# Kernel tuning notes

Hardware: AMD Instinct MI355X
Metric: run time of the kernel (lower is better)

Reference implementation:

```python
import jax, jax.numpy as jnp
import numpy as np

EPS = 1e-12  # tf.contrib layer_norm default epsilon
FORGET_BIAS = 1.0  # tf LSTMCell default


def _layer_norm(x, gamma, beta):
    mu = jnp.mean(x, axis=-1, keepdims=True)
    var = jnp.mean(jnp.square(x - mu), axis=-1, keepdims=True)
    return (x - mu) * jax.lax.rsqrt(var + EPS) * gamma + beta


def setup_inputs() -> dict:
    key = jax.random.key(0)
    ks = jax.random.split(key, 16)
    B, T, OBS, ACT, H = 256, 512, 256, 64, 64
    N = B * T
    s = 0.05
    inp = {
        "obs": jax.random.normal(ks[0], (N, OBS), jnp.float32),
        "action": jax.random.normal(ks[1], (N, ACT), jnp.float32),
        "c0": jnp.zeros((B, H), jnp.float32),
        "h0": jnp.zeros((B, H), jnp.float32),
        "W_obs": jax.random.normal(ks[2], (OBS, H), jnp.float32) * s,
        "b_obs": jnp.zeros((H,), jnp.float32),
        "g1": jnp.ones((H,), jnp.float32),
        "beta1": jnp.zeros((H,), jnp.float32),
        "W_act": jax.random.normal(ks[3], (ACT, H), jnp.float32) * s,
        "b_act": jnp.zeros((H,), jnp.float32),
        "g2": jnp.ones((H,), jnp.float32),
        "beta2": jnp.zeros((H,), jnp.float32),
        "W_lstm": jax.random.normal(ks[4], (2 * H + H, 4 * H), jnp.float32) * s,
        "b_lstm": jnp.zeros((4 * H,), jnp.float32),
        "g3": jnp.ones((H,), jnp.float32),
        "beta3": jnp.zeros((H,), jnp.float32),
        "W_out": jax.random.uniform(ks[5], (H, 1), jnp.float32, -0.003, 0.003),
        "b_out": jnp.zeros((1,), jnp.float32),
        "batch_size": B,
        "step_size": T,
    }
    return inp


def reference(obs, action, c0, h0, W_obs, b_obs, g1, beta1, W_act, b_act, g2, beta2,
              W_lstm, b_lstm, g3, beta3, W_out, b_out, batch_size, step_size):
    H = 64
    # obs branch (output is overwritten below — faithful to source bug)
    x = jnp.maximum(_layer_norm(obs @ W_obs + b_obs, g1, beta1), 0.0)
    # action branch
    yd = action @ W_act + b_act
    x = _layer_norm(yd, g2, beta2)  # BUG in source: overwrites obs branch
    y = jnp.maximum(yd, 0.0)
    xy = jnp.concatenate([x, y], axis=-1)  # [B*T, 128]
    rnn_in = xy.reshape(batch_size, step_size, 2 * H).transpose(1, 0, 2)  # [T,B,128]

    def step(carry, x_t):
        c, h = carry
        z = jnp.concatenate([x_t, h], axis=-1) @ W_lstm + b_lstm  # [B,4H]
        i, j, f, o = jnp.split(z, 4, axis=-1)  # tf LSTMCell gate order
        c_new = c * jax.nn.sigmoid(f + FORGET_BIAS) + jax.nn.sigmoid(i) * jnp.tanh(j)
        h_new = jax.nn.sigmoid(o) * jnp.tanh(c_new)
        return (c_new, h_new), h_new

    (c_fin, h_fin), hs = jax.lax.scan(step, (c0, h0), rnn_in)  # hs: [T,B,H]
    out = hs.transpose(1, 0, 2).reshape(batch_size * step_size, H)
    out = _layer_norm(out, g3, beta3)
    q = out @ W_out + b_out  # [B*T, 1]
    return q, c_fin, h_fin
```

## Files before the change

kernel.cpp:

```cpp
#include <hip/hip_runtime.h>

#define HD 64
#define TT 512
#define BB 256
#define NROWS (BB * TT)

__device__ __forceinline__ float rl(float v, int k) {
  return __uint_as_float(__builtin_amdgcn_readlane(__float_as_uint(v), k));
}
__device__ __forceinline__ float wsum(float v) {
#pragma unroll
  for (int m = 32; m >= 1; m >>= 1) v += __shfl_xor(v, m, 64);
  return v;
}
__device__ __forceinline__ float sigmoidf_(float x) {
  return 1.0f / (1.0f + __expf(-x));
}
__device__ __forceinline__ float tanhf_(float x) {
  return 1.0f - 2.0f / (__expf(2.0f * x) + 1.0f);
}
__device__ __forceinline__ unsigned short f2bf(float f) {
  unsigned int u = __float_as_uint(f);
  u = (u + 0x7fffu + ((u >> 16) & 1u)) >> 16;
  return (unsigned short)u;
}
__device__ __forceinline__ float ldz(const float* p) { return *p; }
__device__ __forceinline__ float ldz(const unsigned short* p) {
  return __uint_as_float(((unsigned int)(*p)) << 16);
}
__device__ __forceinline__ void store8(float* p, float4 a, float4 b) {
  *(float4*)p = a;
  *(float4*)(p + 4) = b;
}
__device__ __forceinline__ void store8(unsigned short* p, float4 a, float4 b) {
  union { unsigned short us[8]; int4 v; } u;
  u.us[0] = f2bf(a.x); u.us[1] = f2bf(a.y); u.us[2] = f2bf(a.z); u.us[3] = f2bf(a.w);
  u.us[4] = f2bf(b.x); u.us[5] = f2bf(b.y); u.us[6] = f2bf(b.z); u.us[7] = f2bf(b.w);
  *(int4*)p = u.v;
}
__device__ __forceinline__ float4 fma4(float4 a, float s, float4 w) {
  a.x += s * w.x; a.y += s * w.y; a.z += s * w.z; a.w += s * w.w;
  return a;
}
__device__ __forceinline__ float4 add4(float4 a, float4 b) {
  a.x += b.x; a.y += b.y; a.z += b.z; a.w += b.w;
  return a;
}

template <typename ZT>
__global__ __launch_bounds__(256) void kA(const float* __restrict__ act,
                                          const float* __restrict__ Wact,
                                          const float* __restrict__ bact,
                                          const float* __restrict__ g2,
                                          const float* __restrict__ beta2,
                                          const float* __restrict__ Wl,
                                          const float* __restrict__ bl,
                                          ZT* __restrict__ Zx) {
  __shared__ float xy[64][128];
  const int tid = threadIdx.x;
  const int lane = tid & 63;
  const int wv = tid >> 6;
  const int r0blk = blockIdx.x * 64;

  float wreg[64];
#pragma unroll
  for (int k = 0; k < 64; ++k) wreg[k] = Wact[k * 64 + lane];
  const float ba = bact[lane], gg = g2[lane], bb = beta2[lane];

  for (int i = 0; i < 16; ++i) {
    const int r = i * 4 + wv;
    const int row = r0blk + r;
    const float a = act[row * 64 + lane];
    float yd = ba;
#pragma unroll
    for (int k = 0; k < 64; ++k) yd += rl(a, k) * wreg[k];
    const float mu = wsum(yd) * (1.0f / 64.0f);
    const float d = yd - mu;
    const float var = wsum(d * d) * (1.0f / 64.0f);
    const float x = d * rsqrtf(var + 1e-12f) * gg + bb;
    xy[r][lane] = x;
    xy[r][64 + lane] = fmaxf(yd, 0.0f);
  }
  __syncthreads();

  const int tc = tid & 31;
  const int tr = tid >> 5;
  const int c0 = tc * 8;
  float4 accA[8], accB[8];
#pragma unroll
  for (int r = 0; r < 8; ++r) {
    accA[r] = make_float4(0.f, 0.f, 0.f, 0.f);
    accB[r] = make_float4(0.f, 0.f, 0.f, 0.f);
  }
  for (int kk = 0; kk < 128; kk += 4) {
    float4 xv[8];
#pragma unroll
    for (int r = 0; r < 8; ++r) xv[r] = *(const float4*)&xy[tr * 8 + r][kk];
#pragma unroll
    for (int dk = 0; dk < 4; ++dk) {
      const float4 wa = *(const float4*)&Wl[(kk + dk) * 256 + c0];
      const float4 wb = *(const float4*)&Wl[(kk + dk) * 256 + c0 + 4];
#pragma unroll
      for (int r = 0; r < 8; ++r) {
        const float xr = (dk == 0) ? xv[r].x : (dk == 1) ? xv[r].y : (dk == 2) ? xv[r].z : xv[r].w;
        accA[r] = fma4(accA[r], xr, wa);
        accB[r] = fma4(accB[r], xr, wb);
      }
    }
  }
  const float4 bla = *(const float4*)&bl[c0];
  const float4 blb = *(const float4*)&bl[c0 + 4];
#pragma unroll
  for (int r = 0; r < 8; ++r) {
    const int row = r0blk + tr * 8 + r;
    store8(&Zx[(size_t)row * 256 + c0], add4(accA[r], bla), add4(accB[r], blb));
  }
}

template <typename ZT>
__global__ __launch_bounds__(256) void kB(const ZT* __restrict__ Zx,
                                          const float* __restrict__ Wl,
                                          const float* __restrict__ c0p,
                                          const float* __restrict__ h0p,
                                          float* __restrict__ hs,
                                          float* __restrict__ cfin,
                                          float* __restrict__ hfin) {
  __shared__ float zbuf[2][256];
  const int tid = threadIdx.x;
  const int m = tid & 63;
  const int b = blockIdx.x;

  float wcol[64];
#pragma unroll
  for (int k = 0; k < 64; ++k) wcol[k] = Wl[(128 + k) * 256 + tid];

  float c = c0p[b * 64 + m];
  float h = h0p[b * 64 + m];

  const ZT* zrow = Zx + (size_t)b * TT * 256;
  float* hsrow = hs + (size_t)b * TT * 64;

  float p0 = ldz(&zrow[0 * 256 + tid]);
  float p1 = ldz(&zrow[1 * 256 + tid]);
  float p2 = ldz(&zrow[2 * 256 + tid]);
  float p3 = ldz(&zrow[3 * 256 + tid]);

#define STEP(PZ, T)                                                        \
  {                                                                        \
    float a0 = 0.f, a1 = 0.f, a2 = 0.f, a3 = 0.f;                          \
    _Pragma("unroll") for (int k = 0; k < 64; k += 4) {                    \
      a0 += rl(h, k) * wcol[k];                                            \
      a1 += rl(h, k + 1) * wcol[k + 1];                                    \
      a2 += rl(h, k + 2) * wcol[k + 2];                                    \
      a3 += rl(h, k + 3) * wcol[k + 3];                                    \
    }                                                                      \
    const float zv = PZ + ((a0 + a1) + (a2 + a3));                         \
    zbuf[(T)&1][tid] = zv;                                                 \
    int tn = (T) + 4;                                                      \
    if (tn > TT - 1) tn = TT - 1;                                          \
    PZ = ldz(&zrow[(size_t)tn * 256 + tid]);                               \
    asm volatile("s_waitcnt lgkmcnt(0)\n\ts_barrier" ::: "memory");        \
    const float zi = zbuf[(T)&1][m];                                       \
    const float zj = zbuf[(T)&1][64 + m];                                  \
    const float zf = zbuf[(T)&1][128 + m];                                 \
    const float zo = zbuf[(T)&1][192 + m];                                 \
    c = c * sigmoidf_(zf + 1.0f) + sigmoidf_(zi) * tanhf_(zj);             \
    h = sigmoidf_(zo) * tanhf_(c);                                         \
    if (tid < 64) hsrow[(T)*64 + m] = h;                                   \
  }

  for (int t = 0; t < TT; t += 4) {
    STEP(p0, t)
    STEP(p1, t + 1)
    STEP(p2, t + 2)
    STEP(p3, t + 3)
  }
#undef STEP

  if (tid < 64) {
    cfin[b * 64 + m] = c;
    hfin[b * 64 + m] = h;
  }
}

__global__ __launch_bounds__(256) void kC(const float* __restrict__ hs,
                                          const float* __restrict__ g3,
                                          const float* __restrict__ beta3,
                                          const float* __restrict__ Wout,
                                          const float* __restrict__ bout,
                                          float* __restrict__ q) {
  const int lane = threadIdx.x & 63;
  const int wv = threadIdx.x >> 6;
  const float g = g3[lane], be = beta3[lane], wo = Wout[lane], bo = bout[0];
  for (int n = blockIdx.x * 4 + wv; n < NROWS; n += gridDim.x * 4) {
    const float v = hs[(size_t)n * 64 + lane];
    const float mu = wsum(v) * (1.0f / 64.0f);
    const float d = v - mu;
    const float var = wsum(d * d) * (1.0f / 64.0f);
    const float xn = d * rsqrtf(var + 1e-12f) * g + be;
    const float s = wsum(xn * wo);
    if (lane == 0) q[n] = s + bo;
  }
}

extern "C" void kernel_launch(void* const* d_in, const int* in_sizes, int n_in,
                              void* d_out, int out_size, void* d_ws, size_t ws_size,
                              hipStream_t stream) {
  const float* action = (const float*)d_in[1];
  const float* c0 = (const float*)d_in[2];
  const float* h0 = (const float*)d_in[3];
  const float* Wact = (const float*)d_in[8];
  const float* bact = (const float*)d_in[9];
  const float* g2 = (const float*)d_in[10];
  const float* b2 = (const float*)d_in[11];
  const float* Wl = (const float*)d_in[12];
  const float* bl = (const float*)d_in[13];
  const float* g3 = (const float*)d_in[14];
  const float* b3 = (const float*)d_in[15];
  const float* Wout = (const float*)d_in[16];
  const float* bout = (const float*)d_in[17];

  float* q = (float*)d_out;
  float* cfin = q + NROWS;
  float* hfin = cfin + BB * HD;

  const size_t zx32 = (size_t)NROWS * 256 * sizeof(float);
  const size_t zx16 = (size_t)NROWS * 256 * sizeof(unsigned short);
  const size_t hsb = (size_t)NROWS * 64 * sizeof(float);

  if (ws_size >= zx32 + hsb) {
    float* Zx = (float*)d_ws;
    float* hs = (float*)((char*)d_ws + zx32);
    kA<float><<<NROWS / 64, 256, 0, stream>>>(action, Wact, bact, g2, b2, Wl, bl, Zx);
    kB<float><<<BB, 256, 0, stream>>>(Zx, Wl, c0, h0, hs, cfin, hfin);
    kC<<<2048, 256, 0, stream>>>(hs, g3, b3, Wout, bout, q);
  } else {
    unsigned short* Zx = (unsigned short*)d_ws;
    float* hs = (float*)((char*)d_ws + zx16);
    kA<unsigned short><<<NROWS / 64, 256, 0, stream>>>(action, Wact, bact, g2, b2, Wl, bl, Zx);
    kB<unsigned short><<<BB, 256, 0, stream>>>(Zx, Wl, c0, h0, hs, cfin, hfin);
    kC<<<2048, 256, 0, stream>>>(hs, g3, b3, Wout, bout, q);
  }
}
```

Baseline: 417.0 us.

## Run LSTM recurrence on one wavefront per batch using bf16 MFMA

The recurrent kernel drops from four wavefronts per batch element, which used readlane dot products and a block barrier each step, to a single wavefront. That wavefront computes the h·W_hh product with bf16 16x16x32 MFMA instructions, with the weights held in registers as bf16 fragments. This removes the cross-wave barrier and LDS gate exchange on the serial critical path. The cost is bf16 rounding of h and the weights, extra MFMAs whose results are mostly discarded (only row 0 is used), and fewer active waves per CU.

```diff
diff --git a/kernel.cpp b/kernel.cpp
--- a/kernel.cpp
+++ b/kernel.cpp
@@ -4,6 +4,9 @@
 #define TT 512
 #define BB 256
 #define NROWS (BB * TT)
+
+typedef __attribute__((ext_vector_type(8))) short short8_t;
+typedef __attribute__((ext_vector_type(4))) float f32x4;
 
 __device__ __forceinline__ float rl(float v, int k) {
   return __uint_as_float(__builtin_amdgcn_readlane(__float_as_uint(v), k));
@@ -118,69 +121,88 @@
 }
 
 template <typename ZT>
-__global__ __launch_bounds__(256) void kB(const ZT* __restrict__ Zx,
+__global__ __launch_bounds__(64) void kB2(const ZT* __restrict__ Zx,
                                           const float* __restrict__ Wl,
                                           const float* __restrict__ c0p,
                                           const float* __restrict__ h0p,
                                           float* __restrict__ hs,
                                           float* __restrict__ cfin,
                                           float* __restrict__ hfin) {
-  __shared__ float zbuf[2][256];
-  const int tid = threadIdx.x;
-  const int m = tid & 63;
+  __shared__ __align__(16) unsigned short h_lds[64];
+  const int l = threadIdx.x;
   const int b = blockIdx.x;
-
-  float wcol[64];
-#pragma unroll
-  for (int k = 0; k < 64; ++k) wcol[k] = Wl[(128 + k) * 256 + tid];
-
-  float c = c0p[b * 64 + m];
-  float h = h0p[b * 64 + m];
+  const int grp = l >> 4;
+  const int col = l & 15;
+
+  short8_t wf0[16], wf1[16];
+#pragma unroll
+  for (int t16 = 0; t16 < 16; ++t16) {
+    short8_t w0, w1;
+#pragma unroll
+    for (int j = 0; j < 8; ++j) {
+      w0[j] = (short)f2bf(Wl[(128 + 0 + grp * 8 + j) * 256 + 16 * t16 + col]);
+      w1[j] = (short)f2bf(Wl[(128 + 32 + grp * 8 + j) * 256 + 16 * t16 + col]);
+    }
+    wf0[t16] = w0;
+    wf1[t16] = w1;
+  }
+
+  const f32x4 zc = {0.f, 0.f, 0.f, 0.f};
+
+  float c = c0p[b * 64 + l];
+  float h = h0p[b * 64 + l];
 
   const ZT* zrow = Zx + (size_t)b * TT * 256;
   float* hsrow = hs + (size_t)b * TT * 64;
 
-  float p0 = ldz(&zrow[0 * 256 + tid]);
-  float p1 = ldz(&zrow[1 * 256 + tid]);
-  float p2 = ldz(&zrow[2 * 256 + tid]);
-  float p3 = ldz(&zrow[3 * 256 + tid]);
-
-#define STEP(PZ, T)                                                        \
-  {                                                                        \
-    float a0 = 0.f, a1 = 0.f, a2 = 0.f, a3 = 0.f;                          \
-    _Pragma("unroll") for (int k = 0; k < 64; k += 4) {                    \
-      a0 += rl(h, k) * wcol[k];                                            \
-      a1 += rl(h, k + 1) * wcol[k + 1];                                    \
-      a2 += rl(h, k + 2) * wcol[k + 2];                                    \
-      a3 += rl(h, k + 3) * wcol[k + 3];                                    \
-    }                                                                      \
-    const float zv = PZ + ((a0 + a1) + (a2 + a3));                         \
-    zbuf[(T)&1][tid] = zv;                                                 \
-    int tn = (T) + 4;                                                      \
-    if (tn > TT - 1) tn = TT - 1;                                          \
-    PZ = ldz(&zrow[(size_t)tn * 256 + tid]);                               \
-    asm volatile("s_waitcnt lgkmcnt(0)\n\ts_barrier" ::: "memory");        \
-    const float zi = zbuf[(T)&1][m];                                       \
-    const float zj = zbuf[(T)&1][64 + m];                                  \
-    const float zf = zbuf[(T)&1][128 + m];                                 \
-    const float zo = zbuf[(T)&1][192 + m];                                 \
-    c = c * sigmoidf_(zf + 1.0f) + sigmoidf_(zi) * tanhf_(zj);             \
-    h = sigmoidf_(zo) * tanhf_(c);                                         \
-    if (tid < 64) hsrow[(T)*64 + m] = h;                                   \
-  }
-
+#define LD4(PI, PJ, PF, PO, T)                       \
+  PI = ldz(&zrow[(size_t)(T) * 256 + 0 + l]);        \
+  PJ = ldz(&zrow[(size_t)(T) * 256 + 64 + l]);       \
+  PF = ldz(&zrow[(size_t)(T) * 256 + 128 + l]);      \
+  PO = ldz(&zrow[(size_t)(T) * 256 + 192 + l]);
+
+  float pAi, pAj, pAf, pAo, pBi, pBj, pBf, pBo;
+  float pCi, pCj, pCf, pCo, pDi, pDj, pDf, pDo;
+  LD4(pAi, pAj, pAf, pAo, 0)
+  LD4(pBi, pBj, pBf, pBo, 1)
+  LD4(pCi, pCj, pCf, pCo, 2)
+  LD4(pDi, pDj, pDf, pDo, 3)
+
+#define STEP(PI, PJ, PF, PO, T)                                               \
+  {                                                                           \
+    h_lds[l] = f2bf(h);                                                       \
+    asm volatile("s_waitcnt lgkmcnt(0)" ::: "memory");                        \
+    const short8_t a0 = *(const short8_t*)&h_lds[grp * 8];                    \
+    const short8_t a1 = *(const short8_t*)&h_lds[32 + grp * 8];               \
+    f32x4 acc[16];                                                            \
+    _Pragma("unroll") for (int t16 = 0; t16 < 16; ++t16) {                    \
+      f32x4 tmp = __builtin_amdgcn_mfma_f32_16x16x32_bf16(a0, wf0[t16], zc, 0, 0, 0); \
+      acc[t16] = __builtin_amdgcn_mfma_f32_16x16x32_bf16(a1, wf1[t16], tmp, 0, 0, 0); \
+    }                                                                         \
+    const float zi = (grp == 0 ? acc[0].x : grp == 1 ? acc[1].x : grp == 2 ? acc[2].x : acc[3].x) + PI;   \
+    const float zj = (grp == 0 ? acc[4].x : grp == 1 ? acc[5].x : grp == 2 ? acc[6].x : acc[7].x) + PJ;   \
+    const float zf = (grp == 0 ? acc[8].x : grp == 1 ? acc[9].x : grp == 2 ? acc[10].x : acc[11].x) + PF; \
+    const float zo = (grp == 0 ? acc[12].x : grp == 1 ? acc[13].x : grp == 2 ? acc[14].x : acc[15].x) + PO; \
+    int tn = (T) + 4;                                                         \
+    if (tn > TT - 1) tn = TT - 1;                                             \
+    LD4(PI, PJ, PF, PO, tn)                                                   \
+    c = c * sigmoidf_(zf + 1.0f) + sigmoidf_(zi) * tanhf_(zj);                \
+    h = sigmoidf_(zo) * tanhf_(c);                                            \
+    hsrow[(size_t)(T) * 64 + l] = h;                                          \
+  }
+
+#pragma unroll 1
   for (int t = 0; t < TT; t += 4) {
-    STEP(p0, t)
-    STEP(p1, t + 1)
-    STEP(p2, t + 2)
-    STEP(p3, t + 3)
+    STEP(pAi, pAj, pAf, pAo, t)
+    STEP(pBi, pBj, pBf, pBo, t + 1)
+    STEP(pCi, pCj, pCf, pCo, t + 2)
+    STEP(pDi, pDj, pDf, pDo, t + 3)
   }
 #undef STEP
-
-  if (tid < 64) {
-    cfin[b * 64 + m] = c;
-    hfin[b * 64 + m] = h;
-  }
+#undef LD4
+
+  cfin[b * 64 + l] = c;
+  hfin[b * 64 + l] = h;
 }
 
 __global__ __launch_bounds__(256) void kC(const float* __restrict__ hs,
@@ -232,13 +254,13 @@
     float* Zx = (float*)d_ws;
     float* hs = (float*)((char*)d_ws + zx32);
     kA<float><<<NROWS / 64, 256, 0, stream>>>(action, Wact, bact, g2, b2, Wl, bl, Zx);
-    kB<float><<<BB, 256, 0, stream>>>(Zx, Wl, c0, h0, hs, cfin, hfin);
+    kB2<float><<<BB, 64, 0, stream>>>(Zx, Wl, c0, h0, hs, cfin, hfin);
     kC<<<2048, 256, 0, stream>>>(hs, g3, b3, Wout, bout, q);
   } else {
     unsigned short* Zx = (unsigned short*)d_ws;
     float* hs = (float*)((char*)d_ws + zx16);
     kA<unsigned short><<<NROWS / 64, 256, 0, stream>>>(action, Wact, bact, g2, b2, Wl, bl, Zx);
-    kB<unsigned short><<<BB, 256, 0, stream>>>(Zx, Wl, c0, h0, hs, cfin, hfin);
+    kB2<unsigned short><<<BB, 64, 0, stream>>>(Zx, Wl, c0, h0, hs, cfin, hfin);
     kC<<<2048, 256, 0, stream>>>(hs, g3, b3, Wout, bout, q);
   }
 }
```

After: 505.3 us. 1.21x slower.

## Run LSTM recurrence on MFMA bf16 with 16 batch rows per block

Applied to the files above, without the earlier changes.

The recurrent kernel is rewritten so each block handles 16 batch rows and computes h@W_h with bf16 16x16x32 MFMA instructions. The recurrent weights are held as bf16 fragments in registers and h is exchanged through a small LDS buffer. The Zx gate preactivations are fed in as the MFMA accumulator input. This replaces the per-batch readlane dot products and cuts the grid from 256 blocks to 16, trading parallelism for matrix-core throughput. Rounding h and W to bf16 adds error that accumulates across the 512 timesteps.

```diff
diff --git a/kernel.cpp b/kernel.cpp
--- a/kernel.cpp
+++ b/kernel.cpp
@@ -4,6 +4,9 @@
 #define TT 512
 #define BB 256
 #define NROWS (BB * TT)
+
+typedef __attribute__((ext_vector_type(8))) short short8_t;
+typedef __attribute__((ext_vector_type(4))) float f32x4;
 
 __device__ __forceinline__ float rl(float v, int k) {
   return __uint_as_float(__builtin_amdgcn_readlane(__float_as_uint(v), k));
@@ -118,68 +121,93 @@
 }
 
 template <typename ZT>
-__global__ __launch_bounds__(256) void kB(const ZT* __restrict__ Zx,
-                                          const float* __restrict__ Wl,
-                                          const float* __restrict__ c0p,
-                                          const float* __restrict__ h0p,
-                                          float* __restrict__ hs,
-                                          float* __restrict__ cfin,
-                                          float* __restrict__ hfin) {
-  __shared__ float zbuf[2][256];
+__global__ __launch_bounds__(256, 1) void kB6(const ZT* __restrict__ Zx,
+                                              const float* __restrict__ Wl,
+                                              const float* __restrict__ c0p,
+                                              const float* __restrict__ h0p,
+                                              float* __restrict__ hs,
+                                              float* __restrict__ cfin,
+                                              float* __restrict__ hfin) {
+  __shared__ __align__(16) unsigned short h_lds[2][16][72];
   const int tid = threadIdx.x;
-  const int m = tid & 63;
-  const int b = blockIdx.x;
-
-  float wcol[64];
-#pragma unroll
-  for (int k = 0; k < 64; ++k) wcol[k] = Wl[(128 + k) * 256 + tid];
-
-  float c = c0p[b * 64 + m];
-  float h = h0p[b * 64 + m];
-
-  const ZT* zrow = Zx + (size_t)b * TT * 256;
-  float* hsrow = hs + (size_t)b * TT * 64;
-
-  float p0 = ldz(&zrow[0 * 256 + tid]);
-  float p1 = ldz(&zrow[1 * 256 + tid]);
-  float p2 = ldz(&zrow[2 * 256 + tid]);
-  float p3 = ldz(&zrow[3 * 256 + tid]);
-
-#define STEP(PZ, T)                                                        \
-  {                                                                        \
-    float a0 = 0.f, a1 = 0.f, a2 = 0.f, a3 = 0.f;                          \
-    _Pragma("unroll") for (int k = 0; k < 64; k += 4) {                    \
-      a0 += rl(h, k) * wcol[k];                                            \
-      a1 += rl(h, k + 1) * wcol[k + 1];                                    \
-      a2 += rl(h, k + 2) * wcol[k + 2];                                    \
-      a3 += rl(h, k + 3) * wcol[k + 3];                                    \
-    }                                                                      \
-    const float zv = PZ + ((a0 + a1) + (a2 + a3));                         \
-    zbuf[(T)&1][tid] = zv;                                                 \
-    int tn = (T) + 4;                                                      \
-    if (tn > TT - 1) tn = TT - 1;                                          \
-    PZ = ldz(&zrow[(size_t)tn * 256 + tid]);                               \
-    asm volatile("s_waitcnt lgkmcnt(0)\n\ts_barrier" ::: "memory");        \
-    const float zi = zbuf[(T)&1][m];                                       \
-    const float zj = zbuf[(T)&1][64 + m];                                  \
-    const float zf = zbuf[(T)&1][128 + m];                                 \
-    const float zo = zbuf[(T)&1][192 + m];                                 \
-    c = c * sigmoidf_(zf + 1.0f) + sigmoidf_(zi) * tanhf_(zj);             \
-    h = sigmoidf_(zo) * tanhf_(c);                                         \
-    if (tid < 64) hsrow[(T)*64 + m] = h;                                   \
-  }
-
+  const int w = tid >> 6;
+  const int l = tid & 63;
+  const int bq = l >> 4;
+  const int cl = l & 15;
+  const int m = w * 16 + cl;
+  const int B0 = blockIdx.x * 16;
+
+  short8_t wf[4][2];
+#pragma unroll
+  for (int g = 0; g < 4; ++g)
+#pragma unroll
+    for (int q = 0; q < 2; ++q) {
+      short8_t v;
+#pragma unroll
+      for (int j = 0; j < 8; ++j)
+        v[j] = (short)f2bf(Wl[(128 + q * 32 + bq * 8 + j) * 256 + g * 64 + w * 16 + cl]);
+      wf[g][q] = v;
+    }
+
+  float c[4], hl[4];
+  size_t zoff[4], hsb[4];
+#pragma unroll
+  for (int r = 0; r < 4; ++r) {
+    const int bl = bq * 4 + r;
+    const int bg = B0 + bl;
+    c[r] = c0p[bg * 64 + m];
+    hl[r] = h0p[bg * 64 + m];
+    h_lds[0][bl][m] = f2bf(hl[r]);
+    zoff[r] = (size_t)bg * TT * 256 + (size_t)(w * 16 + cl);
+    hsb[r] = (size_t)bg * TT * 64 + (size_t)m;
+  }
+  __syncthreads();
+
+  f32x4 P[4][4];
+#define PF(S, T)                                                          \
+  _Pragma("unroll") for (int g = 0; g < 4; ++g)                           \
+  _Pragma("unroll") for (int r = 0; r < 4; ++r)                           \
+      P[S][g][r] = ldz(&Zx[zoff[r] + (size_t)(T) * 256 + g * 64]);
+
+  PF(0, 0) PF(1, 1) PF(2, 2) PF(3, 3)
+
+#define STEP(S, T)                                                                          \
+  {                                                                                         \
+    const short8_t a0 = *(const short8_t*)&h_lds[(T) & 1][cl][bq * 8];                      \
+    const short8_t a1 = *(const short8_t*)&h_lds[(T) & 1][cl][32 + bq * 8];                 \
+    f32x4 acc[4];                                                                           \
+    _Pragma("unroll") for (int g = 0; g < 4; ++g) {                                         \
+      f32x4 t0 = __builtin_amdgcn_mfma_f32_16x16x32_bf16(a0, wf[g][0], P[S][g], 0, 0, 0);   \
+      acc[g] = __builtin_amdgcn_mfma_f32_16x16x32_bf16(a1, wf[g][1], t0, 0, 0, 0);          \
+    }                                                                                       \
+    int tn = (T) + 4;                                                                       \
+    if (tn > TT - 1) tn = TT - 1;                                                           \
+    PF(S, tn)                                                                               \
+    _Pragma("unroll") for (int r = 0; r < 4; ++r) {                                         \
+      const float zi = acc[0][r], zj = acc[1][r], zf = acc[2][r], zo = acc[3][r];           \
+      c[r] = c[r] * sigmoidf_(zf + 1.0f) + sigmoidf_(zi) * tanhf_(zj);                      \
+      hl[r] = sigmoidf_(zo) * tanhf_(c[r]);                                                 \
+      hs[hsb[r] + (size_t)(T) * 64] = hl[r];                                                \
+      h_lds[((T) + 1) & 1][bq * 4 + r][m] = f2bf(hl[r]);                                    \
+    }                                                                                       \
+    __syncthreads();                                                                        \
+  }
+
+#pragma unroll 1
   for (int t = 0; t < TT; t += 4) {
-    STEP(p0, t)
-    STEP(p1, t + 1)
-    STEP(p2, t + 2)
-    STEP(p3, t + 3)
+    STEP(0, t)
+    STEP(1, t + 1)
+    STEP(2, t + 2)
+    STEP(3, t + 3)
   }
 #undef STEP
-
-  if (tid < 64) {
-    cfin[b * 64 + m] = c;
-    hfin[b * 64 + m] = h;
+#undef PF
+
+#pragma unroll
+  for (int r = 0; r < 4; ++r) {
+    const int bg = B0 + bq * 4 + r;
+    cfin[bg * 64 + m] = c[r];
+    hfin[bg * 64 + m] = hl[r];
   }
 }
 
@@ -232,13 +260,13 @@
     float* Zx = (float*)d_ws;
     float* hs = (float*)((char*)d_ws + zx32);
     kA<float><<<NROWS / 64, 256, 0, stream>>>(action, Wact, bact, g2, b2, Wl, bl, Zx);
-    kB<float><<<BB, 256, 0, stream>>>(Zx, Wl, c0, h0, hs, cfin, hfin);
+    kB6<float><<<BB / 16, 256, 0, stream>>>(Zx, Wl, c0, h0, hs, cfin, hfin);
     kC<<<2048, 256, 0, stream>>>(hs, g3, b3, Wout, bout, q);
   } else {
     unsigned short* Zx = (unsigned short*)d_ws;
     float* hs = (float*)((char*)d_ws + zx16);
     kA<unsigned short><<<NROWS / 64, 256, 0, stream>>>(action, Wact, bact, g2, b2, Wl, bl, Zx);
-    kB<unsigned short><<<BB, 256, 0, stream>>>(Zx, Wl, c0, h0, hs, cfin, hfin);
+    kB6<unsigned short><<<BB / 16, 256, 0, stream>>>(Zx, Wl, c0, h0, hs, cfin, hfin);
     kC<<<2048, 256, 0, stream>>>(hs, g3, b3, Wout, bout, q);
   }
 }
```

Result: slower. 712.7 us (+70.9%).
